# Kernel tuning notes

Measured on AMD Instinct MI355X. Metric: run time of the kernel, lower is better.

## Reference

```python
import jax, jax.numpy as jnp
import numpy as np

B, L, D = 2048, 200, 128
HID = [80, 40]


def setup_inputs() -> dict:
    key = jax.random.key(0)
    ks = jax.random.split(key, 10)
    hist_emb = jax.random.normal(ks[0], (B, L, D), dtype=jnp.float32)
    target_emb = jax.random.normal(ks[1], (B, D), dtype=jnp.float32)
    mask = jax.random.randint(ks[2], (B, L), 0, 2, dtype=jnp.int32)
    # MLP params: (4D -> 80 -> 40 -> 1), Kaiming-uniform-ish like nn.Linear default
    dims = [4 * D] + HID + [1]
    params = {}
    for i in range(len(dims) - 1):
        fan_in = dims[i]
        bound = 1.0 / np.sqrt(fan_in)
        params[f"W{i}"] = jax.random.uniform(ks[3 + 2 * i], (dims[i], dims[i + 1]), minval=-bound, maxval=bound, dtype=jnp.float32)
        params[f"b{i}"] = jax.random.uniform(ks[4 + 2 * i], (dims[i + 1],), minval=-bound, maxval=bound, dtype=jnp.float32)
    return {"hist_emb": hist_emb, "target_emb": target_emb, "mask": mask, **params}


def reference(hist_emb, target_emb, mask, W0, b0, W1, b1, W2, b2):
    # hist_emb: (B,L,D); target_emb: (B,D); mask: (B,L)
    target = target_emb[:, None, :]                       # (B,1,D) -> broadcast over L
    diff = hist_emb - target
    prod = hist_emb * target
    tgt = jnp.broadcast_to(target, hist_emb.shape)
    feat = jnp.concatenate([hist_emb, tgt, diff, prod], axis=-1)  # (B,L,4D)
    h = jax.nn.relu(jnp.einsum("blf,fh->blh", feat, W0) + b0)
    h = jax.nn.relu(jnp.einsum("blf,fh->blh", h, W1) + b1)
    scores = (jnp.einsum("blf,fh->blh", h, W2) + b2)[..., 0]      # (B,L)
    m = mask.astype(scores.dtype)
    logits = scores + (1.0 - m) * -1e9
    attn = jax.nn.softmax(logits, axis=1)                 # (B,L)
    user_interest = jnp.einsum("bl,bld->bd", attn, hist_emb)
    return user_interest, attn
```

## Files before the change

### kernel.cpp

```cpp
#include <hip/hip_runtime.h>
#include <hip/hip_bf16.h>

#define B_  2048
#define L_  200
#define D_  128
#define H0_ 80
#define H1_ 40
#define NT_ 25600

typedef __attribute__((ext_vector_type(8))) short short8;
typedef __attribute__((ext_vector_type(4))) float floatx4;

__device__ __forceinline__ short f2bf(float f) {
    unsigned u = __float_as_uint(f);
    u += 0x7fffu + ((u >> 16) & 1u);
    return (short)(u >> 16);
}
__device__ __forceinline__ float bf2f(short s) {
    return __uint_as_float(((unsigned)(unsigned short)s) << 16);
}

#define W1T_SOFF  20480
#define BEFF_FOFF 12544

__global__ __launch_bounds__(256, 2) void prep_kernel(
    const float* __restrict__ tgt, const float* __restrict__ W0,
    const float* __restrict__ b0, const float* __restrict__ W1,
    short* __restrict__ Bg, short* __restrict__ w1t, float* __restrict__ beff2)
{
    __shared__ short w0bc[D_][84];
    __shared__ float tgs[D_];
    __shared__ float red3[3][H0_];

    const int tid = threadIdx.x;
    for (int i = tid; i < D_ * H0_; i += 256) {
        int d = i / H0_, h = i - d * H0_;
        w0bc[d][h] = f2bf(W0[128 * H0_ + i] - W0[256 * H0_ + i]);
    }
    if (blockIdx.x == 0) {
        for (int i = tid; i < H0_ * 256; i += 256) {
            int h = i >> 8, k = i & 255;
            float v = (k < 128) ? (W0[k * H0_ + h] + W0[(256 + k) * H0_ + h])
                                : W0[(384 + (k - 128)) * H0_ + h];
            Bg[i] = f2bf(v);
        }
        for (int i = tid; i < 48 * 96; i += 256) {
            int n = i / 96, k = i - n * 96;
            w1t[i] = (n < H1_ && k < H0_) ? f2bf(W1[k * H1_ + n]) : (short)0;
        }
    }
    for (int bb = 0; bb < 8; ++bb) {
        const int b = blockIdx.x * 8 + bb;
        __syncthreads();
        if (tid < D_) tgs[tid] = tgt[(size_t)b * D_ + tid];
        __syncthreads();
        if (tid < 240) {
            int seg = tid / H0_, h = tid - seg * H0_;
            int d0 = seg * 43, d1 = (seg == 2) ? D_ : d0 + 43;
            float s = 0.f;
            #pragma unroll 8
            for (int d = d0; d < d1; ++d) s += tgs[d] * bf2f(w0bc[d][h]);
            red3[seg][h] = s;
        }
        __syncthreads();
        if (tid < H0_)
            beff2[(size_t)b * H0_ + tid] = b0[tid] + red3[0][tid] + red3[1][tid] + red3[2][tid];
    }
}

__global__ __launch_bounds__(256, 2) void score_kernel(
    const float* __restrict__ hist, const float* __restrict__ tgt,
    const short* __restrict__ Bg, const short* __restrict__ w1t,
    const float* __restrict__ beff2, const float* __restrict__ b1,
    const float* __restrict__ W2, const float* __restrict__ b2,
    float* __restrict__ out)
{
    __shared__ __align__(16) short Bs[H0_][264];
    __shared__ __align__(16) short h0t[4][16][104];

    const int tid = threadIdx.x;
    const int wave = tid >> 6, lane = tid & 63;
    const int col = lane & 15, quad = lane >> 4;

    for (int i = tid; i < 2560; i += 256) {
        int h = i >> 5, k0 = (i & 31) * 8;
        *(short8*)&Bs[h][k0] = *(const short8*)(Bg + (h << 8) + k0);
    }
    if (tid < 192) {
        int w = tid / 48, rem = tid % 48, row = rem / 3, c = 80 + (rem % 3) * 8;
        *(short8*)&h0t[w][row][c] = (short8)0;
    }
    __syncthreads();

    short8 w1f[3][3];
    #pragma unroll
    for (int ks = 0; ks < 3; ++ks)
        #pragma unroll
        for (int nt = 0; nt < 3; ++nt)
            w1f[ks][nt] = *(const short8*)(w1t + (nt * 16 + col) * 96 + ks * 32 + quad * 8);
    float b1r[3], w2r[3];
    #pragma unroll
    for (int nt = 0; nt < 3; ++nt) {
        int h = nt * 16 + col;
        b1r[nt] = (h < H1_) ? b1[h] : 0.f;
        w2r[nt] = (h < H1_) ? W2[h] : 0.f;
    }
    const float b2v = b2[0];

    const int wid = blockIdx.x * 4 + wave;

    for (int it = 0; it < 7; ++it) {
        const int tile = wid * 7 + it;
        if (tile >= NT_) break;
        const int row = tile * 16 + col;
        const int bl  = row / 200u;
        const float* ap = hist + (size_t)row * D_ + quad * 8;
        const float* tp = tgt + (size_t)bl * D_ + quad * 8;

        floatx4 A[8], T[8];
        #pragma unroll
        for (int u = 0; u < 8; ++u) A[u] = *(const floatx4*)(ap + (u >> 1) * 32 + (u & 1) * 4);
        #pragma unroll
        for (int u = 0; u < 8; ++u) T[u] = *(const floatx4*)(tp + (u >> 1) * 32 + (u & 1) * 4);

        const int rowq = tile * 16 + quad * 4;
        float beffr[5][4];
        {
            int bq0 = rowq / 200u, bq3 = (rowq + 3) / 200u;
            if (bq0 == bq3) {
                #pragma unroll
                for (int nt = 0; nt < 5; ++nt) {
                    float v = beff2[(size_t)bq0 * H0_ + nt * 16 + col];
                    #pragma unroll
                    for (int r = 0; r < 4; ++r) beffr[nt][r] = v;
                }
            } else {
                #pragma unroll
                for (int r = 0; r < 4; ++r) {
                    int br = (rowq + r) / 200u;
                    #pragma unroll
                    for (int nt = 0; nt < 5; ++nt)
                        beffr[nt][r] = beff2[(size_t)br * H0_ + nt * 16 + col];
                }
            }
        }

        short8 ah[4], ag[4];
        #pragma unroll
        for (int ks = 0; ks < 4; ++ks) {
            short8 h8, g8;
            #pragma unroll
            for (int j = 0; j < 8; ++j) {
                float hv = A[2 * ks + (j >> 2)][j & 3];
                float tv = T[2 * ks + (j >> 2)][j & 3];
                h8[j] = f2bf(hv);
                g8[j] = f2bf(hv * tv);
            }
            ah[ks] = h8; ag[ks] = g8;
        }

        floatx4 c0[5];
        #pragma unroll
        for (int nt = 0; nt < 5; ++nt) c0[nt] = (floatx4)0.f;
        #pragma unroll
        for (int ks = 0; ks < 4; ++ks)
            #pragma unroll
            for (int nt = 0; nt < 5; ++nt) {
                short8 bfr = *(const short8*)&Bs[nt * 16 + col][ks * 32 + quad * 8];
                c0[nt] = __builtin_amdgcn_mfma_f32_16x16x32_bf16(ah[ks], bfr, c0[nt], 0, 0, 0);
            }
        #pragma unroll
        for (int ks = 0; ks < 4; ++ks)
            #pragma unroll
            for (int nt = 0; nt < 5; ++nt) {
                short8 bfr = *(const short8*)&Bs[nt * 16 + col][128 + ks * 32 + quad * 8];
                c0[nt] = __builtin_amdgcn_mfma_f32_16x16x32_bf16(ag[ks], bfr, c0[nt], 0, 0, 0);
            }

        #pragma unroll
        for (int nt = 0; nt < 5; ++nt)
            #pragma unroll
            for (int r = 0; r < 4; ++r) {
                float v = c0[nt][r] + beffr[nt][r];
                v = v > 0.f ? v : 0.f;
                h0t[wave][quad * 4 + r][nt * 16 + col] = f2bf(v);
            }

        floatx4 c1[3];
        #pragma unroll
        for (int nt = 0; nt < 3; ++nt) c1[nt] = (floatx4)0.f;
        #pragma unroll
        for (int ks = 0; ks < 3; ++ks) {
            short8 a1 = *(const short8*)&h0t[wave][col][ks * 32 + quad * 8];
            #pragma unroll
            for (int nt = 0; nt < 3; ++nt)
                c1[nt] = __builtin_amdgcn_mfma_f32_16x16x32_bf16(a1, w1f[ks][nt], c1[nt], 0, 0, 0);
        }

        float s4[4] = {0.f, 0.f, 0.f, 0.f};
        #pragma unroll
        for (int nt = 0; nt < 3; ++nt)
            #pragma unroll
            for (int r = 0; r < 4; ++r) {
                float v = c1[nt][r] + b1r[nt];
                v = v > 0.f ? v : 0.f;
                s4[r] += v * w2r[nt];
            }
        #pragma unroll
        for (int r = 0; r < 4; ++r) {
            s4[r] += __shfl_xor(s4[r], 1, 16);
            s4[r] += __shfl_xor(s4[r], 2, 16);
            s4[r] += __shfl_xor(s4[r], 4, 16);
            s4[r] += __shfl_xor(s4[r], 8, 16);
        }
        if (col == 0) {
            #pragma unroll
            for (int r = 0; r < 4; ++r)
                out[(size_t)B_ * D_ + rowq + r] = s4[r] + b2v;
        }
    }
}

__global__ __launch_bounds__(256, 8) void attn_kernel(
    const float* __restrict__ hist, const int* __restrict__ mask,
    float* __restrict__ out)
{
    __shared__ float attns[L_];
    __shared__ float red[8];
    __shared__ float p0[D_];
    __shared__ float p1[D_];

    const int tid = threadIdx.x;
    const int b   = blockIdx.x;
    float* attn_out = out + (size_t)B_ * D_ + (size_t)b * L_;
    float* ui_out   = out + (size_t)b * D_;

    float sc = -3.0e38f;
    if (tid < L_) {
        sc = attn_out[tid];
        if (mask[(size_t)b * L_ + tid] == 0) sc -= 1e9f;
    }
    float m = sc;
    #pragma unroll
    for (int off = 32; off >= 1; off >>= 1) m = fmaxf(m, __shfl_xor(m, off, 64));
    int wid = tid >> 6;
    if ((tid & 63) == 0) red[wid] = m;
    __syncthreads();
    m = fmaxf(fmaxf(red[0], red[1]), fmaxf(red[2], red[3]));
    float e = (tid < L_) ? __expf(sc - m) : 0.f;
    float s = e;
    #pragma unroll
    for (int off = 32; off >= 1; off >>= 1) s += __shfl_xor(s, off, 64);
    if ((tid & 63) == 0) red[4 + wid] = s;
    __syncthreads();
    s = red[4] + red[5] + red[6] + red[7];
    float inv = 1.0f / s;
    float av = e * inv;
    if (tid < L_) {
        attns[tid] = av;
        attn_out[tid] = av;
    }
    __syncthreads();

    const int half = tid >> 7, d = tid & 127;
    const float* hb = hist + ((size_t)b * L_ + half * 100) * D_ + d;
    float acc = 0.f;
    #pragma unroll 25
    for (int l = 0; l < 100; ++l)
        acc = fmaf(attns[half * 100 + l], hb[(size_t)l * D_], acc);
    if (half) p1[d] = acc; else p0[d] = acc;
    __syncthreads();
    if (tid < D_) ui_out[tid] = p0[tid] + p1[tid];
}

extern "C" void kernel_launch(void* const* d_in, const int* in_sizes, int n_in,
                              void* d_out, int out_size, void* d_ws, size_t ws_size,
                              hipStream_t stream) {
    const float* hist = (const float*)d_in[0];
    const float* tgt  = (const float*)d_in[1];
    const int*   mask = (const int*)d_in[2];
    const float* W0   = (const float*)d_in[3];
    const float* b0   = (const float*)d_in[4];
    const float* W1   = (const float*)d_in[5];
    const float* b1   = (const float*)d_in[6];
    const float* W2   = (const float*)d_in[7];
    const float* b2   = (const float*)d_in[8];

    short* Bg    = (short*)d_ws;
    short* w1t   = (short*)d_ws + W1T_SOFF;
    float* beff2 = (float*)d_ws + BEFF_FOFF;

    prep_kernel<<<256, 256, 0, stream>>>(tgt, W0, b0, W1, Bg, w1t, beff2);
    score_kernel<<<1024, 256, 0, stream>>>(hist, tgt, Bg, w1t, beff2, b1, W2, b2,
                                           (float*)d_out);
    attn_kernel<<<B_, 256, 0, stream>>>(hist, mask, (float*)d_out);
}
```

Measured before the change: 391.2 us.

## Fuse score MLP, softmax and weighted sum into one per-batch kernel

Merges the score and attention kernels into a single kernel where each block handles four batch rows: it computes the per-batch effective bias in shared memory, runs the MFMA MLP over padded 16-row tiles, keeps the scores in LDS, then does the softmax and attention-weighted sum. This removes the global round trip of the scores, one kernel launch and the per-batch bias workspace. The second read of hist for the weighted sum now likely hits cache. The cost is padded tiles (208 rows for 200), extra block syncs, and 512 blocks where there used to be 1024.

```diff
diff --git a/kernel.cpp b/kernel.cpp
--- a/kernel.cpp
+++ b/kernel.cpp
@@ -6,7 +6,14 @@
 #define D_  128
 #define H0_ 80
 #define H1_ 40
-#define NT_ 25600
+#define BPB 4
+#define NTILE 13
+#define TT_ (BPB*NTILE)
+
+#define WS_BG  0
+#define WS_W1T 20480
+#define WS_W0P 25088
+#define WS_TOT 35840
 
 typedef __attribute__((ext_vector_type(8))) short short8;
 typedef __attribute__((ext_vector_type(4))) float floatx4;
@@ -20,84 +27,89 @@
     return __uint_as_float(((unsigned)(unsigned short)s) << 16);
 }
 
-#define W1T_SOFF  20480
-#define BEFF_FOFF 12544
-
-__global__ __launch_bounds__(256, 2) void prep_kernel(
-    const float* __restrict__ tgt, const float* __restrict__ W0,
-    const float* __restrict__ b0, const float* __restrict__ W1,
-    short* __restrict__ Bg, short* __restrict__ w1t, float* __restrict__ beff2)
+__global__ __launch_bounds__(256) void prep_kernel(
+    const float* __restrict__ W0, const float* __restrict__ W1,
+    short* __restrict__ ws)
 {
-    __shared__ short w0bc[D_][84];
-    __shared__ float tgs[D_];
-    __shared__ float red3[3][H0_];
-
-    const int tid = threadIdx.x;
-    for (int i = tid; i < D_ * H0_; i += 256) {
-        int d = i / H0_, h = i - d * H0_;
-        w0bc[d][h] = f2bf(W0[128 * H0_ + i] - W0[256 * H0_ + i]);
-    }
-    if (blockIdx.x == 0) {
-        for (int i = tid; i < H0_ * 256; i += 256) {
+    for (int i = blockIdx.x * 256 + threadIdx.x; i < WS_TOT; i += 64 * 256) {
+        short v;
+        if (i < WS_W1T) {
             int h = i >> 8, k = i & 255;
-            float v = (k < 128) ? (W0[k * H0_ + h] + W0[(256 + k) * H0_ + h])
-                                : W0[(384 + (k - 128)) * H0_ + h];
-            Bg[i] = f2bf(v);
-        }
-        for (int i = tid; i < 48 * 96; i += 256) {
-            int n = i / 96, k = i - n * 96;
-            w1t[i] = (n < H1_ && k < H0_) ? f2bf(W1[k * H1_ + n]) : (short)0;
-        }
-    }
-    for (int bb = 0; bb < 8; ++bb) {
-        const int b = blockIdx.x * 8 + bb;
-        __syncthreads();
-        if (tid < D_) tgs[tid] = tgt[(size_t)b * D_ + tid];
-        __syncthreads();
-        if (tid < 240) {
-            int seg = tid / H0_, h = tid - seg * H0_;
-            int d0 = seg * 43, d1 = (seg == 2) ? D_ : d0 + 43;
-            float s = 0.f;
-            #pragma unroll 8
-            for (int d = d0; d < d1; ++d) s += tgs[d] * bf2f(w0bc[d][h]);
-            red3[seg][h] = s;
-        }
-        __syncthreads();
-        if (tid < H0_)
-            beff2[(size_t)b * H0_ + tid] = b0[tid] + red3[0][tid] + red3[1][tid] + red3[2][tid];
-    }
-}
-
-__global__ __launch_bounds__(256, 2) void score_kernel(
+            float x = (k < 128) ? (W0[(size_t)k * H0_ + h] + W0[(size_t)(256 + k) * H0_ + h])
+                                : W0[(size_t)(384 + (k - 128)) * H0_ + h];
+            v = f2bf(x);
+        } else if (i < WS_W0P) {
+            int j = i - WS_W1T;
+            int n = j / 96, k = j - n * 96;
+            v = (n < H1_ && k < H0_) ? f2bf(W1[(size_t)k * H1_ + n]) : (short)0;
+        } else {
+            int j = i - WS_W0P;
+            int d = j / 84, h = j - d * 84;
+            v = (h < H0_) ? f2bf(W0[(size_t)(128 + d) * H0_ + h] - W0[(size_t)(256 + d) * H0_ + h])
+                          : (short)0;
+        }
+        ws[i] = v;
+    }
+}
+
+__global__ __launch_bounds__(256, 2) void fused_kernel(
     const float* __restrict__ hist, const float* __restrict__ tgt,
-    const short* __restrict__ Bg, const short* __restrict__ w1t,
-    const float* __restrict__ beff2, const float* __restrict__ b1,
+    const int* __restrict__ mask, const short* __restrict__ ws,
+    const float* __restrict__ b0p, const float* __restrict__ b1,
     const float* __restrict__ W2, const float* __restrict__ b2,
     float* __restrict__ out)
 {
     __shared__ __align__(16) short Bs[H0_][264];
     __shared__ __align__(16) short h0t[4][16][104];
+    __shared__ float tgs4[BPB][D_];
+    __shared__ float beffs[BPB][H0_];
+    __shared__ float scores4[BPB][208];
+    __shared__ float red[8];
+    __shared__ float p0[D_], p1[D_];
 
     const int tid = threadIdx.x;
     const int wave = tid >> 6, lane = tid & 63;
     const int col = lane & 15, quad = lane >> 4;
+    const int bbase = blockIdx.x * BPB;
+
+    short* w0s = &Bs[0][0];
+    float* red3 = &scores4[0][0];
+
+    for (int i = tid; i < 1344; i += 256)
+        *(short8*)(w0s + i * 8) = *(const short8*)(ws + WS_W0P + i * 8);
+    for (int i = tid; i < BPB * D_; i += 256)
+        tgs4[i >> 7][i & 127] = tgt[(size_t)(bbase + (i >> 7)) * D_ + (i & 127)];
+    __syncthreads();
+
+    for (int bb = 0; bb < BPB; ++bb) {
+        if (tid < 240) {
+            int seg = tid / 80, h = tid - seg * 80;
+            int d0 = seg * 43, d1 = (seg == 2) ? D_ : d0 + 43;
+            float s = 0.f;
+            #pragma unroll 8
+            for (int d = d0; d < d1; ++d) s += tgs4[bb][d] * bf2f(w0s[d * 84 + h]);
+            red3[seg * H0_ + h] = s;
+        }
+        __syncthreads();
+        if (tid < H0_)
+            beffs[bb][tid] = b0p[tid] + red3[tid] + red3[H0_ + tid] + red3[2 * H0_ + tid];
+        __syncthreads();
+    }
 
     for (int i = tid; i < 2560; i += 256) {
         int h = i >> 5, k0 = (i & 31) * 8;
-        *(short8*)&Bs[h][k0] = *(const short8*)(Bg + (h << 8) + k0);
+        *(short8*)&Bs[h][k0] = *(const short8*)(ws + WS_BG + (h << 8) + k0);
     }
     if (tid < 192) {
         int w = tid / 48, rem = tid % 48, row = rem / 3, c = 80 + (rem % 3) * 8;
         *(short8*)&h0t[w][row][c] = (short8)0;
     }
-    __syncthreads();
-
     short8 w1f[3][3];
     #pragma unroll
     for (int ks = 0; ks < 3; ++ks)
         #pragma unroll
         for (int nt = 0; nt < 3; ++nt)
-            w1f[ks][nt] = *(const short8*)(w1t + (nt * 16 + col) * 96 + ks * 32 + quad * 8);
+            w1f[ks][nt] = *(const short8*)(ws + WS_W1T + (nt * 16 + col) * 96 + ks * 32 + quad * 8);
     float b1r[3], w2r[3];
     #pragma unroll
     for (int nt = 0; nt < 3; ++nt) {
@@ -106,44 +118,20 @@
         w2r[nt] = (h < H1_) ? W2[h] : 0.f;
     }
     const float b2v = b2[0];
-
-    const int wid = blockIdx.x * 4 + wave;
-
-    for (int it = 0; it < 7; ++it) {
-        const int tile = wid * 7 + it;
-        if (tile >= NT_) break;
-        const int row = tile * 16 + col;
-        const int bl  = row / 200u;
-        const float* ap = hist + (size_t)row * D_ + quad * 8;
-        const float* tp = tgt + (size_t)bl * D_ + quad * 8;
-
-        floatx4 A[8], T[8];
+    __syncthreads();
+
+    for (int tt = wave; tt < TT_; tt += 4) {
+        const int bb = tt / NTILE, t = tt - bb * NTILE;
+        const int l = t * 16 + col;
+        const int lc = (l < L_) ? l : (L_ - 1);
+        const float* ap = hist + ((size_t)(bbase + bb) * L_ + lc) * D_ + quad * 8;
+
+        floatx4 A[8], T8[8];
         #pragma unroll
         for (int u = 0; u < 8; ++u) A[u] = *(const floatx4*)(ap + (u >> 1) * 32 + (u & 1) * 4);
         #pragma unroll
-        for (int u = 0; u < 8; ++u) T[u] = *(const floatx4*)(tp + (u >> 1) * 32 + (u & 1) * 4);
-
-        const int rowq = tile * 16 + quad * 4;
-        float beffr[5][4];
-        {
-            int bq0 = rowq / 200u, bq3 = (rowq + 3) / 200u;
-            if (bq0 == bq3) {
-                #pragma unroll
-                for (int nt = 0; nt < 5; ++nt) {
-                    float v = beff2[(size_t)bq0 * H0_ + nt * 16 + col];
-                    #pragma unroll
-                    for (int r = 0; r < 4; ++r) beffr[nt][r] = v;
-                }
-            } else {
-                #pragma unroll
-                for (int r = 0; r < 4; ++r) {
-                    int br = (rowq + r) / 200u;
-                    #pragma unroll
-                    for (int nt = 0; nt < 5; ++nt)
-                        beffr[nt][r] = beff2[(size_t)br * H0_ + nt * 16 + col];
-                }
-            }
-        }
+        for (int u = 0; u < 8; ++u)
+            T8[u] = *(const floatx4*)&tgs4[bb][quad * 8 + (u >> 1) * 32 + (u & 1) * 4];
 
         short8 ah[4], ag[4];
         #pragma unroll
@@ -152,7 +140,7 @@
             #pragma unroll
             for (int j = 0; j < 8; ++j) {
                 float hv = A[2 * ks + (j >> 2)][j & 3];
-                float tv = T[2 * ks + (j >> 2)][j & 3];
+                float tv = T8[2 * ks + (j >> 2)][j & 3];
                 h8[j] = f2bf(hv);
                 g8[j] = f2bf(hv * tv);
             }
@@ -178,13 +166,15 @@
             }
 
         #pragma unroll
-        for (int nt = 0; nt < 5; ++nt)
+        for (int nt = 0; nt < 5; ++nt) {
+            float be = beffs[bb][nt * 16 + col];
             #pragma unroll
             for (int r = 0; r < 4; ++r) {
-                float v = c0[nt][r] + beffr[nt][r];
+                float v = c0[nt][r] + be;
                 v = v > 0.f ? v : 0.f;
                 h0t[wave][quad * 4 + r][nt * 16 + col] = f2bf(v);
             }
+        }
 
         floatx4 c1[3];
         #pragma unroll
@@ -216,61 +206,49 @@
         if (col == 0) {
             #pragma unroll
             for (int r = 0; r < 4; ++r)
-                out[(size_t)B_ * D_ + rowq + r] = s4[r] + b2v;
-        }
-    }
-}
-
-__global__ __launch_bounds__(256, 8) void attn_kernel(
-    const float* __restrict__ hist, const int* __restrict__ mask,
-    float* __restrict__ out)
-{
-    __shared__ float attns[L_];
-    __shared__ float red[8];
-    __shared__ float p0[D_];
-    __shared__ float p1[D_];
-
-    const int tid = threadIdx.x;
-    const int b   = blockIdx.x;
-    float* attn_out = out + (size_t)B_ * D_ + (size_t)b * L_;
-    float* ui_out   = out + (size_t)b * D_;
-
-    float sc = -3.0e38f;
-    if (tid < L_) {
-        sc = attn_out[tid];
-        if (mask[(size_t)b * L_ + tid] == 0) sc -= 1e9f;
-    }
-    float m = sc;
-    #pragma unroll
-    for (int off = 32; off >= 1; off >>= 1) m = fmaxf(m, __shfl_xor(m, off, 64));
-    int wid = tid >> 6;
-    if ((tid & 63) == 0) red[wid] = m;
+                scores4[bb][t * 16 + quad * 4 + r] = s4[r] + b2v;
+        }
+    }
     __syncthreads();
-    m = fmaxf(fmaxf(red[0], red[1]), fmaxf(red[2], red[3]));
-    float e = (tid < L_) ? __expf(sc - m) : 0.f;
-    float s = e;
-    #pragma unroll
-    for (int off = 32; off >= 1; off >>= 1) s += __shfl_xor(s, off, 64);
-    if ((tid & 63) == 0) red[4 + wid] = s;
-    __syncthreads();
-    s = red[4] + red[5] + red[6] + red[7];
-    float inv = 1.0f / s;
-    float av = e * inv;
-    if (tid < L_) {
-        attns[tid] = av;
-        attn_out[tid] = av;
-    }
-    __syncthreads();
-
-    const int half = tid >> 7, d = tid & 127;
-    const float* hb = hist + ((size_t)b * L_ + half * 100) * D_ + d;
-    float acc = 0.f;
-    #pragma unroll 25
-    for (int l = 0; l < 100; ++l)
-        acc = fmaf(attns[half * 100 + l], hb[(size_t)l * D_], acc);
-    if (half) p1[d] = acc; else p0[d] = acc;
-    __syncthreads();
-    if (tid < D_) ui_out[tid] = p0[tid] + p1[tid];
+
+    for (int bb = 0; bb < BPB; ++bb) {
+        const int b = bbase + bb;
+
+        float sc = -3.0e38f;
+        if (tid < L_) {
+            sc = scores4[bb][tid];
+            if (mask[(size_t)b * L_ + tid] == 0) sc -= 1e9f;
+        }
+        float m = sc;
+        #pragma unroll
+        for (int off = 32; off >= 1; off >>= 1) m = fmaxf(m, __shfl_xor(m, off, 64));
+        if (lane == 0) red[wave] = m;
+        __syncthreads();
+        m = fmaxf(fmaxf(red[0], red[1]), fmaxf(red[2], red[3]));
+        float e = (tid < L_) ? __expf(sc - m) : 0.f;
+        float s = e;
+        #pragma unroll
+        for (int off = 32; off >= 1; off >>= 1) s += __shfl_xor(s, off, 64);
+        if (lane == 0) red[4 + wave] = s;
+        __syncthreads();
+        s = red[4] + red[5] + red[6] + red[7];
+        float av = e * (1.0f / s);
+        if (tid < L_) {
+            scores4[bb][tid] = av;
+            out[(size_t)B_ * D_ + (size_t)b * L_ + tid] = av;
+        }
+        __syncthreads();
+
+        const int half = tid >> 7, d = tid & 127;
+        const float* hb = hist + ((size_t)b * L_ + half * 100) * D_ + d;
+        float acc = 0.f;
+        #pragma unroll 25
+        for (int l = 0; l < 100; ++l)
+            acc = fmaf(scores4[bb][half * 100 + l], hb[(size_t)l * D_], acc);
+        if (half) p1[d] = acc; else p0[d] = acc;
+        __syncthreads();
+        if (tid < D_) out[(size_t)b * D_ + tid] = p0[tid] + p1[tid];
+    }
 }
 
 extern "C" void kernel_launch(void* const* d_in, const int* in_sizes, int n_in,
@@ -286,12 +264,9 @@
     const float* W2   = (const float*)d_in[7];
     const float* b2   = (const float*)d_in[8];
 
-    short* Bg    = (short*)d_ws;
-    short* w1t   = (short*)d_ws + W1T_SOFF;
-    float* beff2 = (float*)d_ws + BEFF_FOFF;
-
-    prep_kernel<<<256, 256, 0, stream>>>(tgt, W0, b0, W1, Bg, w1t, beff2);
-    score_kernel<<<1024, 256, 0, stream>>>(hist, tgt, Bg, w1t, beff2, b1, W2, b2,
-                                           (float*)d_out);
-    attn_kernel<<<B_, 256, 0, stream>>>(hist, mask, (float*)d_out);
-}
+    short* ws = (short*)d_ws;
+
+    prep_kernel<<<64, 256, 0, stream>>>(W0, W1, ws);
+    fused_kernel<<<B_ / BPB, 256, 0, stream>>>(hist, tgt, mask, ws, b0, b1, W2, b2,
+                                               (float*)d_out);
+}
```

Measured after the change: 362.1 us. -7.4%, faster.
